# Optimization experiments

Measured on AMD Instinct MI355X. Metric: run time of the kernel, lower is better.

The kernel has to match this reference:

```python
import jax, jax.numpy as jnp
import numpy as np

B, T, D, M, L = 4, 2048, 256, 128, 16
P = M * L  # max_pair_cnt


def setup_inputs() -> dict:
    key = jax.random.key(0)
    ks = jax.random.split(key, 11)
    head = jax.random.normal(ks[0], (B, P, T), jnp.float32) * 0.05
    tail = jax.random.normal(ks[1], (B, P, T), jnp.float32) * 0.05
    x = jax.random.normal(ks[2], (B, T, D), jnp.float32)
    coref_mention_position = jax.random.uniform(ks[3], (B, M, T), jnp.float32)
    lab = jax.random.uniform(ks[4], (B, P, 2), jnp.float32) + 1e-3
    coref_label = lab / lab.sum(-1, keepdims=True)  # already-softmaxed target
    coref_label_mask = jax.random.randint(ks[5], (B, P), 0, 2).astype(bool)
    lens = jnp.full((B, M), L, jnp.int32)  # uniform segment lengths
    w1 = jax.random.normal(ks[6], (3 * D, D), jnp.float32) / np.sqrt(3 * D).astype(np.float32)
    b1 = jnp.zeros((D,), jnp.float32)
    w2 = jax.random.normal(ks[7], (D, 2), jnp.float32) / np.sqrt(D).astype(np.float32)
    b2 = jnp.zeros((2,), jnp.float32)
    return {"head": head, "tail": tail, "lens": lens, "x": x,
            "coref_mention_position": coref_mention_position,
            "coref_label": coref_label, "coref_label_mask": coref_label_mask,
            "w1": w1, "b1": b1, "w2": w2, "b2": b2}


def reference(head, tail, lens, x, coref_mention_position, coref_label,
              coref_label_mask, w1, b1, w2, b2):
    # bmm-based gather of mention reps: [B,P,T] @ [B,T,D] -> [B,P,D]
    head_rep = jnp.einsum('bpt,btd->bpd', head, x)
    tail_rep = jnp.einsum('bpt,btd->bpd', tail, x)
    feat = jnp.concatenate([head_rep, tail_rep, head_rep * tail_rep], axis=-1)
    logits = jax.nn.relu(feat @ w1 + b1) @ w2 + b2  # [B,P,2]

    # ragged split_n_pad -> per-mention top-1 select (uniform lens == L -> reshape)
    scores = logits[..., 1].reshape(B, M, L)            # [B,M,L]
    max_idx = jnp.argmax(scores, axis=-1)               # [B,M]
    max_val = jnp.max(scores, axis=-1)                  # [B,M] (raw logit, as in source)
    tail_seg = tail_rep.reshape(B, M, L, D)
    sel = jnp.take_along_axis(tail_seg, max_idx[:, :, None, None], axis=2)[:, :, 0, :]
    coref_rep_m = sel * max_val[:, :, None]             # [B,M,D]

    # scatter-bmm merge back into sequence: [B,T,M] @ [B,M,D] -> [B,T,D]
    coref_rep = jnp.einsum('bmt,bmd->btd', coref_mention_position, coref_rep_m)
    output = x + coref_rep

    # KLDivLoss(reduction='mean') over masked pairs
    logq = jax.nn.log_softmax(logits, axis=-1)
    lab = coref_label
    pw = jnp.where(lab > 0, lab * jnp.log(jnp.maximum(lab, 1e-38)), 0.0) - lab * logq
    n = jnp.sum(coref_label_mask).astype(jnp.float32)
    loss = jnp.where(coref_label_mask[..., None], pw, 0.0).sum() / (n * 2.0)
    return output, loss
```

## Files before the change

### kernel.cpp

```cpp
#include <hip/hip_runtime.h>
#include <hip/hip_bf16.h>
#include <stdint.h>

#define TAU 0.35f

typedef __attribute__((ext_vector_type(8))) short bf16x8;
typedef __attribute__((ext_vector_type(4))) float f32x4;

__device__ __forceinline__ unsigned short f2bf(float f) {
  __bf16 h = (__bf16)f;
  return __builtin_bit_cast(unsigned short, h);
}
__device__ __forceinline__ float bf2f(unsigned short u) {
  unsigned int v = ((unsigned int)u) << 16;
  return __builtin_bit_cast(float, v);
}
__device__ __forceinline__ void async_copy16(const void* g, void* l) {
  __builtin_amdgcn_global_load_lds(
      (const __attribute__((address_space(1))) unsigned int*)g,
      (__attribute__((address_space(3))) unsigned int*)l, 16, 0, 0);
}

__global__ __launch_bounds__(256) void k_prep(
    const float* __restrict__ x, const float* __restrict__ w1,
    const float* __restrict__ b2,
    unsigned short* __restrict__ xt, unsigned short* __restrict__ w1t,
    float* __restrict__ logits, int* __restrict__ njobs) {
  __shared__ float tileS[64][65];
  __shared__ float tx[64][132];
  int bx = blockIdx.x, tid = threadIdx.x;
  if (bx == 0 && tid == 0) *njobs = 0;
  if (bx < 64) {
    int i = bx * 256 + tid;
    logits[i] = b2[i & 1];
  }
  if (bx < 256) {
    int b = bx >> 6, kc = (bx >> 1) & 31, dh = bx & 1;
    const float* src = x + ((size_t)b * 2048 + (size_t)kc * 64) * 256 + dh * 128;
#pragma unroll
    for (int p = 0; p < 8; ++p) {
      int idx = p * 256 + tid;
      int row = idx >> 5, f4 = idx & 31;
      *(float4*)&tx[row][f4 * 4] = *(const float4*)&src[(size_t)row * 256 + f4 * 4];
    }
    __syncthreads();
    unsigned short* dst = xt + ((size_t)(b * 32 + kc)) * 16384 + dh * 1024;
#pragma unroll
    for (int p = 0; p < 4; ++p) {
      int idx = p * 256 + tid;
      int d0 = idx & 127, k8 = idx >> 7;
      bf16x8 v;
#pragma unroll
      for (int j = 0; j < 8; ++j) v[j] = (short)f2bf(tx[k8 * 8 + j][d0]);
      *(bf16x8*)&dst[(size_t)k8 * 2048 + d0 * 8] = v;
    }
  } else {
    int wt = bx - 256;
    int k6 = wt >> 2, n6 = wt & 3;
    int j = tid & 63, i0 = tid >> 6;
    const float* src = w1 + ((size_t)k6 * 64) * 256 + n6 * 64;
    for (int i = i0; i < 64; i += 4) tileS[i][j] = src[(size_t)i * 256 + j];
    __syncthreads();
    unsigned short* dst = w1t + ((size_t)n6 * 64) * 768 + k6 * 64;
    for (int r = i0; r < 64; r += 4) dst[(size_t)r * 768 + j] = f2bf(tileS[j][r]);
  }
}

__global__ __launch_bounds__(512, 4) void k_gemm_rep(
    const float* __restrict__ head, const float* __restrict__ tail,
    const unsigned short* __restrict__ xt,
    float* __restrict__ hrep, float* __restrict__ trep) {
  __shared__ unsigned short As[2][2048];
  __shared__ unsigned short Bs[2][16384];
  int bx = blockIdx.x;
  int b = bx >> 7, mt = bx & 127;
  const float* Asrc = ((mt < 64) ? head : tail) +
                      ((size_t)(b * 2048 + (mt & 63) * 32)) * 2048;
  float* Crep = (mt < 64) ? hrep : trep;
  const unsigned short* Bsrc = xt + (size_t)b * 524288;

  int tid = threadIdx.x, lane = tid & 63, w = tid >> 6;
  int rg = w & 1, cg = w >> 1;
  int l4 = lane >> 4, l15 = lane & 15;

  int arow = tid >> 3, ak8 = tid & 7;
  const float* aptr = Asrc + (size_t)arow * 2048 + ak8 * 8;
  int awi = (ak8 * 32 + arow) * 8;

  const unsigned short* bg = Bsrc + tid * 8;

  int aoff[2];
  int boff[2][4];
#pragma unroll
  for (int kh = 0; kh < 2; ++kh) {
    aoff[kh] = ((kh * 4 + l4) * 32 + rg * 16 + l15) * 8;
#pragma unroll
    for (int ct = 0; ct < 4; ++ct)
      boff[kh][ct] = ((kh * 4 + l4) * 256 + cg * 64 + ct * 16 + l15) * 8;
  }

  f32x4 acc[4];
#pragma unroll
  for (int ct = 0; ct < 4; ++ct) acc[ct] = (f32x4){0.f, 0.f, 0.f, 0.f};

  float4 av0, av1;
  auto STAGEB = [&](int buf) {
#pragma unroll
    for (int a = 0; a < 4; ++a)
      async_copy16(bg + (size_t)a * 4096, &Bs[buf][(tid + a * 512) * 8]);
    bg += 16384;
  };
  auto LOADA = [&]() {
    const float4* ap = (const float4*)aptr;
    av0 = ap[0]; av1 = ap[1];
    aptr += 64;
  };
  auto WRITEA = [&](int buf) {
    bf16x8 p;
    p[0] = (short)f2bf(av0.x); p[1] = (short)f2bf(av0.y);
    p[2] = (short)f2bf(av0.z); p[3] = (short)f2bf(av0.w);
    p[4] = (short)f2bf(av1.x); p[5] = (short)f2bf(av1.y);
    p[6] = (short)f2bf(av1.z); p[7] = (short)f2bf(av1.w);
    *(bf16x8*)&As[buf][awi] = p;
  };
  auto MMA = [&](int buf) {
    const unsigned short* A_ = As[buf];
    const unsigned short* B_ = Bs[buf];
#pragma unroll
    for (int kh = 0; kh < 2; ++kh) {
      bf16x8 a0 = *(const bf16x8*)&A_[aoff[kh]];
#pragma unroll
      for (int ct = 0; ct < 4; ++ct) {
        bf16x8 bb = *(const bf16x8*)&B_[boff[kh][ct]];
        acc[ct] = __builtin_amdgcn_mfma_f32_16x16x32_bf16(a0, bb, acc[ct], 0, 0, 0);
      }
    }
  };

  STAGEB(0);
  if (tid < 256) { LOADA(); WRITEA(0); }
  __syncthreads();

  for (int it = 0; it < 32; ++it) {
    int cur = it & 1, nxt = cur ^ 1;
    if (it < 31) {
      STAGEB(nxt);
      if (tid < 256) LOADA();
    }
    MMA(cur);
    if (it < 31 && tid < 256) WRITEA(nxt);
    __syncthreads();
  }

  size_t prow = (size_t)b * 2048 + (size_t)(mt & 63) * 32 + rg * 16 + (l4 << 2);
  int cb = cg * 64 + l15;
#pragma unroll
  for (int ct = 0; ct < 4; ++ct)
#pragma unroll
    for (int i = 0; i < 4; ++i)
      Crep[(prow + i) * 256 + cb + ct * 16] = acc[ct][i];
}

__global__ __launch_bounds__(256) void k_feat(
    const float* __restrict__ hrep, const float* __restrict__ trep,
    unsigned short* __restrict__ featbf) {
  int gid = blockIdx.x * 256 + threadIdx.x;
  int p = gid >> 6, d0 = (gid & 63) * 4;
  float4 h4 = *(const float4*)&hrep[(size_t)p * 256 + d0];
  float4 t4 = *(const float4*)&trep[(size_t)p * 256 + d0];
  ushort4 a, bb, c;
  a.x = f2bf(h4.x); a.y = f2bf(h4.y); a.z = f2bf(h4.z); a.w = f2bf(h4.w);
  bb.x = f2bf(t4.x); bb.y = f2bf(t4.y); bb.z = f2bf(t4.z); bb.w = f2bf(t4.w);
  c.x = f2bf(h4.x * t4.x); c.y = f2bf(h4.y * t4.y);
  c.z = f2bf(h4.z * t4.z); c.w = f2bf(h4.w * t4.w);
  *(ushort4*)&featbf[(size_t)p * 768 + d0] = a;
  *(ushort4*)&featbf[(size_t)p * 768 + 256 + d0] = bb;
  *(ushort4*)&featbf[(size_t)p * 768 + 512 + d0] = c;
}

__global__ __launch_bounds__(256, 4) void k_gemm_mlp(
    const unsigned short* __restrict__ featb, const unsigned short* __restrict__ w1t,
    const float* __restrict__ b1, const float* __restrict__ w2,
    float* __restrict__ logits) {
  __shared__ unsigned short As[2][4096], Bs[2][4096];
  int bx = blockIdx.x;
  int ntile = bx >> 7;
  int mtile = bx & 127;
  int tid = threadIdx.x, lane = tid & 63, w = tid >> 6;

  const unsigned short* ag[2];
  const unsigned short* bgp[2];
  int dofs[2];
#pragma unroll
  for (int a = 0; a < 2; ++a) {
    int rowofs = a * 8 + (lane >> 3);
    int k8 = (lane & 7) ^ (rowofs & 7);
    ag[a] = featb + (size_t)(mtile * 64 + w * 16 + rowofs) * 768 + k8 * 8;
    bgp[a] = w1t + (size_t)(ntile * 64 + w * 16 + rowofs) * 768 + k8 * 8;
    dofs[a] = (w * 128 + a * 64 + lane) * 8;
  }
  int sw0 = (lane >> 4) ^ (lane & 7);
  int sw1 = (4 + (lane >> 4)) ^ (lane & 7);
  int arowc = (w * 16 + (lane & 15)) * 8;
  int colc[4];
#pragma unroll
  for (int ct = 0; ct < 4; ++ct) colc[ct] = (ct * 16 + (lane & 15)) * 8;

  f32x4 acc[4];
#pragma unroll
  for (int ct = 0; ct < 4; ++ct) acc[ct] = (f32x4){0.f, 0.f, 0.f, 0.f};

#pragma unroll
  for (int a = 0; a < 2; ++a) {
    async_copy16(ag[a], &As[0][dofs[a]]); ag[a] += 64;
    async_copy16(bgp[a], &Bs[0][dofs[a]]); bgp[a] += 64;
  }
  __syncthreads();

  for (int it = 0; it < 12; ++it) {
    int cur = it & 1, nxt = cur ^ 1;
    if (it < 11) {
#pragma unroll
      for (int a = 0; a < 2; ++a) {
        async_copy16(ag[a], &As[nxt][dofs[a]]); ag[a] += 64;
        async_copy16(bgp[a], &Bs[nxt][dofs[a]]); bgp[a] += 64;
      }
    }
    const unsigned short* A_ = As[cur];
    const unsigned short* B_ = Bs[cur];
    bf16x8 a0 = *(const bf16x8*)&A_[(arowc + sw0) * 8];
    bf16x8 a1 = *(const bf16x8*)&A_[(arowc + sw1) * 8];
#pragma unroll
    for (int ct = 0; ct < 4; ++ct) {
      bf16x8 b0 = *(const bf16x8*)&B_[(colc[ct] + sw0) * 8];
      acc[ct] = __builtin_amdgcn_mfma_f32_16x16x32_bf16(a0, b0, acc[ct], 0, 0, 0);
    }
#pragma unroll
    for (int ct = 0; ct < 4; ++ct) {
      bf16x8 b1 = *(const bf16x8*)&B_[(colc[ct] + sw1) * 8];
      acc[ct] = __builtin_amdgcn_mfma_f32_16x16x32_bf16(a1, b1, acc[ct], 0, 0, 0);
    }
    __syncthreads();
  }

  float bv[4], w20[4], w21[4];
#pragma unroll
  for (int ct = 0; ct < 4; ++ct) {
    int col = ntile * 64 + ct * 16 + (lane & 15);
    bv[ct] = b1[col]; w20[ct] = w2[col * 2]; w21[ct] = w2[col * 2 + 1];
  }
#pragma unroll
  for (int i = 0; i < 4; ++i) {
    float s0 = 0.f, s1 = 0.f;
#pragma unroll
    for (int ct = 0; ct < 4; ++ct) {
      float r = fmaxf(acc[ct][i] + bv[ct], 0.f);
      s0 += r * w20[ct]; s1 += r * w21[ct];
    }
#pragma unroll
    for (int off = 1; off < 16; off <<= 1) {
      s0 += __shfl_xor(s0, off); s1 += __shfl_xor(s1, off);
    }
    if ((lane & 15) == 0) {
      int row = mtile * 64 + w * 16 + ((lane >> 4) << 2) + i;
      atomicAdd(&logits[row * 2], s0);
      atomicAdd(&logits[row * 2 + 1], s1);
    }
  }
}

__global__ void k_select(const float* __restrict__ logits, int* __restrict__ idxv,
                         float* __restrict__ mval, int* __restrict__ cmask,
                         int* __restrict__ njobs, int* __restrict__ jobs) {
  int q = blockIdx.x * 256 + threadIdx.x;
  if (q >= 512) return;
  int base = q * 16;
  float s[16];
#pragma unroll
  for (int i = 0; i < 16; ++i) s[i] = logits[(size_t)(base + i) * 2 + 1];
  float best = s[0]; int bi = 0;
#pragma unroll
  for (int i = 1; i < 16; ++i) if (s[i] > best) { best = s[i]; bi = i; }
  int mask = 0, cnt = 0;
#pragma unroll
  for (int i = 0; i < 16; ++i) if (s[i] > best - TAU) { mask |= 1 << i; ++cnt; }
  idxv[q] = bi; mval[q] = best;
  if (cnt > 1) {
    cmask[q] = mask;
    for (int i = 0; i < 16; ++i)
      if ((mask >> i) & 1) { int j = atomicAdd(njobs, 1); jobs[j] = base + i; }
  } else cmask[q] = 0;
}

__global__ __launch_bounds__(1024) void k_refine(
    const int* __restrict__ njobs, const int* __restrict__ jobs,
    const float* __restrict__ head, const float* __restrict__ tail,
    const float* __restrict__ x, const float* __restrict__ w1,
    const float* __restrict__ b1, const float* __restrict__ w2,
    const float* __restrict__ b2, float* __restrict__ refined) {
  __shared__ float hrow[2048], trow[2048], feat[768], red[1024], red2[1024];
  int tid = threadIdx.x, seg = tid >> 8, d = tid & 255;
  int nj = *njobs;
  for (int job = blockIdx.x; job < nj; job += gridDim.x) {
    int code = jobs[job];
    int b = code >> 11, p = code & 2047;
    if (tid < 512)
      *(float4*)&hrow[tid * 4] = *(const float4*)&head[((size_t)(b * 2048 + p)) * 2048 + tid * 4];
    else {
      int u = tid - 512;
      *(float4*)&trow[u * 4] = *(const float4*)&tail[((size_t)(b * 2048 + p)) * 2048 + u * 4];
    }
    __syncthreads();
    float hr = 0.f, tr = 0.f;
    const float* xb = x + ((size_t)b * 2048) * 256 + d;
#pragma unroll 8
    for (int t = seg * 512; t < seg * 512 + 512; ++t) {
      float xv = xb[(size_t)t * 256];
      hr += hrow[t] * xv; tr += trow[t] * xv;
    }
    red[tid] = hr; red2[tid] = tr;
    __syncthreads();
    if (seg == 0) {
      float fh = red[d] + red[256 + d] + red[512 + d] + red[768 + d];
      float ft = red2[d] + red2[256 + d] + red2[512 + d] + red2[768 + d];
      feat[d] = fh; feat[256 + d] = ft; feat[512 + d] = fh * ft;
    }
    __syncthreads();
    float hp = 0.f;
    for (int ii = seg * 192; ii < seg * 192 + 192; ++ii) hp += feat[ii] * w1[(size_t)ii * 256 + d];
    red[tid] = hp;
    __syncthreads();
    if (seg == 0) {
      float hj = b1[d] + red[d] + red[256 + d] + red[512 + d] + red[768 + d];
      hj = fmaxf(hj, 0.f);
      red2[d] = hj * w2[d * 2 + 1];
    }
    __syncthreads();
    for (int s = 128; s > 0; s >>= 1) {
      if (tid < s) red2[tid] += red2[tid + s];
      __syncthreads();
    }
    if (tid == 0) refined[code] = red2[0] + b2[1];
    __syncthreads();
  }
}

__global__ __launch_bounds__(256) void k_repm(
    const int* __restrict__ idxv, const float* __restrict__ mval,
    const int* __restrict__ cmask, const float* __restrict__ refined,
    const float* __restrict__ trep, float* __restrict__ repm) {
  int q = blockIdx.x, d = threadIdx.x;
  int mask = cmask[q]; int bi; float v;
  if (mask) {
    bi = -1; v = -1e30f;
    for (int i = 0; i < 16; ++i)
      if ((mask >> i) & 1) { float s = refined[q * 16 + i]; if (s > v) { v = s; bi = i; } }
  } else { bi = idxv[q]; v = mval[q]; }
  repm[(size_t)q * 256 + d] = trep[((size_t)q * 16 + bi) * 256 + d] * v;
}

__global__ __launch_bounds__(256) void k_merge(
    const float* __restrict__ cmp, const float* __restrict__ repm,
    const float* __restrict__ x, float* __restrict__ out) {
  __shared__ float cl[128 * 16];
  int bx = blockIdx.x, b = bx >> 7, t0 = (bx & 127) * 16;
  int tid = threadIdx.x;
#pragma unroll
  for (int it = 0; it < 2; ++it) {
    int f = it * 256 + tid;
    int row = f >> 2, c4 = (f & 3) * 4;
    *(float4*)&cl[row * 16 + c4] =
        *(const float4*)&cmp[((size_t)(b * 128 + row)) * 2048 + t0 + c4];
  }
  __syncthreads();
  float acc[16];
#pragma unroll
  for (int i = 0; i < 16; ++i) acc[i] = 0.f;
  int d = tid;
  for (int m = 0; m < 128; ++m) {
    float rv = repm[(size_t)(b * 128 + m) * 256 + d];
    const float4* c4p = (const float4*)&cl[m * 16];
#pragma unroll
    for (int jj = 0; jj < 4; ++jj) {
      float4 c = c4p[jj];
      acc[jj * 4] += c.x * rv; acc[jj * 4 + 1] += c.y * rv;
      acc[jj * 4 + 2] += c.z * rv; acc[jj * 4 + 3] += c.w * rv;
    }
  }
  const float* xb = x + ((size_t)(b * 2048 + t0)) * 256 + d;
  float* ob = out + ((size_t)(b * 2048 + t0)) * 256 + d;
#pragma unroll
  for (int tt = 0; tt < 16; ++tt) ob[(size_t)tt * 256] = xb[(size_t)tt * 256] + acc[tt];
}

__global__ __launch_bounds__(1024) void k_loss(
    const float* __restrict__ logits, const float* __restrict__ lab,
    const unsigned char* __restrict__ mask, float* __restrict__ out_loss) {
  __shared__ float rs[1024], rc[1024];
  int tid = threadIdx.x;
  float sum = 0.f, cnt = 0.f;
  for (int p = tid; p < 8192; p += 1024) {
    float l0 = logits[(size_t)p * 2], l1 = logits[(size_t)p * 2 + 1];
    float a0 = lab[(size_t)p * 2], a1 = lab[(size_t)p * 2 + 1];
    float mx = fmaxf(l0, l1);
    float lse = mx + logf(expf(l0 - mx) + expf(l1 - mx));
    float pw = 0.f;
    if (a0 > 0.f) pw += a0 * logf(fmaxf(a0, 1e-38f));
    if (a1 > 0.f) pw += a1 * logf(fmaxf(a1, 1e-38f));
    pw -= a0 * (l0 - lse) + a1 * (l1 - lse);
    if (mask[p]) { sum += pw; cnt += 1.f; }
  }
  rs[tid] = sum; rc[tid] = cnt;
  __syncthreads();
  for (int s = 512; s > 0; s >>= 1) {
    if (tid < s) { rs[tid] += rs[tid + s]; rc[tid] += rc[tid + s]; }
    __syncthreads();
  }
  if (tid == 0) *out_loss = rs[0] / (rc[0] * 2.0f);
}

extern "C" void kernel_launch(void* const* d_in, const int* in_sizes, int n_in,
                              void* d_out, int out_size, void* d_ws, size_t ws_size,
                              hipStream_t stream) {
  (void)in_sizes; (void)n_in; (void)out_size; (void)ws_size;
  const float* head = (const float*)d_in[0];
  const float* tail = (const float*)d_in[1];
  const float* x = (const float*)d_in[3];
  const float* cmp = (const float*)d_in[4];
  const float* lab = (const float*)d_in[5];
  const unsigned char* lmask = (const unsigned char*)d_in[6];
  const float* w1 = (const float*)d_in[7];
  const float* b1 = (const float*)d_in[8];
  const float* w2 = (const float*)d_in[9];
  const float* b2 = (const float*)d_in[10];
  float* out = (float*)d_out;

  char* ws = (char*)d_ws;
  size_t off = 0;
  auto alloc = [&](size_t bytes) -> void* {
    void* p = ws + off; off += (bytes + 255) & ~(size_t)255; return p;
  };
  unsigned short* xt = (unsigned short*)alloc(4ull * 256 * 2048 * 2);
  unsigned short* w1t = (unsigned short*)alloc(256ull * 768 * 2);
  float* hrep = (float*)alloc(8192ull * 256 * 4);
  float* trep = (float*)alloc(8192ull * 256 * 4);
  unsigned short* featb = (unsigned short*)alloc(8192ull * 768 * 2);
  float* logits = (float*)alloc(8192ull * 2 * 4);
  float* refined = (float*)alloc(8192ull * 4);
  int* idxv = (int*)alloc(512 * 4);
  float* mvalv = (float*)alloc(512 * 4);
  int* cmaskv = (int*)alloc(512 * 4);
  int* njobs = (int*)alloc(256);
  int* jobs = (int*)alloc(8192 * 4);
  float* repm = (float*)alloc(512ull * 256 * 4);

  k_prep<<<304, 256, 0, stream>>>(x, w1, b2, xt, w1t, logits, njobs);
  k_gemm_rep<<<512, 512, 0, stream>>>(head, tail, xt, hrep, trep);
  k_feat<<<2048, 256, 0, stream>>>(hrep, trep, featb);
  k_gemm_mlp<<<512, 256, 0, stream>>>(featb, w1t, b1, w2, logits);
  k_select<<<2, 256, 0, stream>>>(logits, idxv, mvalv, cmaskv, njobs, jobs);
  k_refine<<<256, 1024, 0, stream>>>(njobs, jobs, head, tail, x, w1, b1, w2, b2, refined);
  k_repm<<<512, 256, 0, stream>>>(idxv, mvalv, cmaskv, refined, trep, repm);
  k_merge<<<512, 256, 0, stream>>>(cmp, repm, x, out);
  k_loss<<<1, 1024, 0, stream>>>(logits, lab, lmask, out + 4ull * 2048 * 256);
}
```

Measured before the change: 315.6 us.

## Batch four refine jobs per block to reuse x and w1 loads

```diff
diff --git a/kernel.cpp b/kernel.cpp
--- a/kernel.cpp
+++ b/kernel.cpp
@@ -29,7 +29,7 @@
   __shared__ float tileS[64][65];
   __shared__ float tx[64][132];
   int bx = blockIdx.x, tid = threadIdx.x;
-  if (bx == 0 && tid == 0) *njobs = 0;
+  if (bx == 0 && tid < 4) njobs[tid] = 0;
   if (bx < 64) {
     int i = bx * 256 + tid;
     logits[i] = b2[i & 1];
@@ -287,61 +287,110 @@
   idxv[q] = bi; mval[q] = best;
   if (cnt > 1) {
     cmask[q] = mask;
+    int bb = q >> 7;
     for (int i = 0; i < 16; ++i)
-      if ((mask >> i) & 1) { int j = atomicAdd(njobs, 1); jobs[j] = base + i; }
+      if ((mask >> i) & 1) {
+        int j = atomicAdd(&njobs[bb], 1);
+        jobs[bb * 2048 + j] = base + i;
+      }
   } else cmask[q] = 0;
 }
 
+#define JPB 4
 __global__ __launch_bounds__(1024) void k_refine(
     const int* __restrict__ njobs, const int* __restrict__ jobs,
     const float* __restrict__ head, const float* __restrict__ tail,
     const float* __restrict__ x, const float* __restrict__ w1,
     const float* __restrict__ b1, const float* __restrict__ w2,
     const float* __restrict__ b2, float* __restrict__ refined) {
-  __shared__ float hrow[2048], trow[2048], feat[768], red[1024], red2[1024];
-  int tid = threadIdx.x, seg = tid >> 8, d = tid & 255;
-  int nj = *njobs;
-  for (int job = blockIdx.x; job < nj; job += gridDim.x) {
-    int code = jobs[job];
-    int b = code >> 11, p = code & 2047;
-    if (tid < 512)
-      *(float4*)&hrow[tid * 4] = *(const float4*)&head[((size_t)(b * 2048 + p)) * 2048 + tid * 4];
-    else {
-      int u = tid - 512;
-      *(float4*)&trow[u * 4] = *(const float4*)&tail[((size_t)(b * 2048 + p)) * 2048 + u * 4];
-    }
-    __syncthreads();
-    float hr = 0.f, tr = 0.f;
-    const float* xb = x + ((size_t)b * 2048) * 256 + d;
+  __shared__ float rows4[2048][8];
+  __shared__ float redH[8][4][256];
+  __shared__ float redT[8][4][256];
+  __shared__ float feat4[768][4];
+  __shared__ float part[4][4];
+  __shared__ int scode[4];
+  int tid = threadIdx.x;
+  int tseg = tid >> 7, dp = tid & 127;
+  int hseg = tid >> 8, d = tid & 255;
+
+  for (int b = 0; b < 4; ++b) {
+    int nj = njobs[b];
+    int ng = (nj + JPB - 1) / JPB;
+    const float* xb = x + (size_t)b * 2048 * 256;
+    for (int grp = blockIdx.x; grp < ng; grp += gridDim.x) {
+      if (tid < 4) scode[tid] = jobs[b * 2048 + min(grp * JPB + tid, nj - 1)];
+      __syncthreads();
+#pragma unroll
+      for (int r = 0; r < 16; ++r) {
+        int idx = r * 1024 + tid;
+        int t = idx >> 3, j = idx & 7;
+        int p = scode[j & 3] & 2047;
+        const float* src = (j < 4) ? head : tail;
+        ((float*)rows4)[idx] = src[((size_t)(b * 2048 + p)) * 2048 + t];
+      }
+      __syncthreads();
+      float2 hr[4], tr[4];
+#pragma unroll
+      for (int j = 0; j < 4; ++j) { hr[j] = {0.f, 0.f}; tr[j] = {0.f, 0.f}; }
+      const float* xp = xb + (size_t)(tseg * 256) * 256 + dp * 2;
 #pragma unroll 8
-    for (int t = seg * 512; t < seg * 512 + 512; ++t) {
-      float xv = xb[(size_t)t * 256];
-      hr += hrow[t] * xv; tr += trow[t] * xv;
-    }
-    red[tid] = hr; red2[tid] = tr;
-    __syncthreads();
-    if (seg == 0) {
-      float fh = red[d] + red[256 + d] + red[512 + d] + red[768 + d];
-      float ft = red2[d] + red2[256 + d] + red2[512 + d] + red2[768 + d];
-      feat[d] = fh; feat[256 + d] = ft; feat[512 + d] = fh * ft;
-    }
-    __syncthreads();
-    float hp = 0.f;
-    for (int ii = seg * 192; ii < seg * 192 + 192; ++ii) hp += feat[ii] * w1[(size_t)ii * 256 + d];
-    red[tid] = hp;
-    __syncthreads();
-    if (seg == 0) {
-      float hj = b1[d] + red[d] + red[256 + d] + red[512 + d] + red[768 + d];
-      hj = fmaxf(hj, 0.f);
-      red2[d] = hj * w2[d * 2 + 1];
-    }
-    __syncthreads();
-    for (int s = 128; s > 0; s >>= 1) {
-      if (tid < s) red2[tid] += red2[tid + s];
-      __syncthreads();
-    }
-    if (tid == 0) refined[code] = red2[0] + b2[1];
-    __syncthreads();
+      for (int t = 0; t < 256; ++t) {
+        float2 xv = *(const float2*)(xp + (size_t)t * 256);
+        float4 hv = *(const float4*)&rows4[tseg * 256 + t][0];
+        float4 tv = *(const float4*)&rows4[tseg * 256 + t][4];
+        hr[0].x += hv.x * xv.x; hr[0].y += hv.x * xv.y;
+        hr[1].x += hv.y * xv.x; hr[1].y += hv.y * xv.y;
+        hr[2].x += hv.z * xv.x; hr[2].y += hv.z * xv.y;
+        hr[3].x += hv.w * xv.x; hr[3].y += hv.w * xv.y;
+        tr[0].x += tv.x * xv.x; tr[0].y += tv.x * xv.y;
+        tr[1].x += tv.y * xv.x; tr[1].y += tv.y * xv.y;
+        tr[2].x += tv.z * xv.x; tr[2].y += tv.z * xv.y;
+        tr[3].x += tv.w * xv.x; tr[3].y += tv.w * xv.y;
+      }
+#pragma unroll
+      for (int j = 0; j < 4; ++j) {
+        *(float2*)&redH[tseg][j][dp * 2] = hr[j];
+        *(float2*)&redT[tseg][j][dp * 2] = tr[j];
+      }
+      __syncthreads();
+      if (tid < 256) {
+#pragma unroll
+        for (int j = 0; j < 4; ++j) {
+          float fh = 0.f, ft = 0.f;
+#pragma unroll
+          for (int s = 0; s < 8; ++s) { fh += redH[s][j][tid]; ft += redT[s][j][tid]; }
+          feat4[tid][j] = fh; feat4[256 + tid][j] = ft; feat4[512 + tid][j] = fh * ft;
+        }
+      }
+      __syncthreads();
+      float hp[4] = {0.f, 0.f, 0.f, 0.f};
+      const float* w1c = w1 + (size_t)(hseg * 192) * 256 + d;
+#pragma unroll 4
+      for (int ii = 0; ii < 192; ++ii) {
+        float wv = w1c[(size_t)ii * 256];
+        float4 fv = *(const float4*)&feat4[hseg * 192 + ii][0];
+        hp[0] += fv.x * wv; hp[1] += fv.y * wv; hp[2] += fv.z * wv; hp[3] += fv.w * wv;
+      }
+#pragma unroll
+      for (int j = 0; j < 4; ++j) redH[hseg][j][d] = hp[j];
+      __syncthreads();
+      if (tid < 256) {
+        float w2v = w2[tid * 2 + 1];
+        float b1v = b1[tid];
+#pragma unroll
+        for (int j = 0; j < 4; ++j) {
+          float h = b1v + redH[0][j][tid] + redH[1][j][tid] + redH[2][j][tid] + redH[3][j][tid];
+          h = fmaxf(h, 0.f) * w2v;
+#pragma unroll
+          for (int off = 1; off < 64; off <<= 1) h += __shfl_xor(h, off);
+          if ((tid & 63) == 0) part[j][tid >> 6] = h;
+        }
+      }
+      __syncthreads();
+      if (tid < 4)
+        refined[scode[tid]] = part[tid][0] + part[tid][1] + part[tid][2] + part[tid][3] + b2[1];
+      __syncthreads();
+    }
   }
 }
 
@@ -451,7 +500,7 @@
   float* mvalv = (float*)alloc(512 * 4);
   int* cmaskv = (int*)alloc(512 * 4);
   int* njobs = (int*)alloc(256);
-  int* jobs = (int*)alloc(8192 * 4);
+  int* jobs = (int*)alloc(4 * 2048 * 4);
   float* repm = (float*)alloc(512ull * 256 * 4);
 
   k_prep<<<304, 256, 0, stream>>>(x, w1, b2, xt, w1t, logits, njobs);
```

Measured after the change: 632.2 us. 2x slower.
